# Performance work log

Hardware: AMD Instinct MI355X
Metric: run time of the kernel (lower is better)

Reference implementation:

```python
import jax, jax.numpy as jnp
import numpy as np

B, T, D = 32, 1024, 1024
PCA_DIM = 256
NS = 4
NC = 1024
SEC = PCA_DIM // NS


def setup_inputs() -> dict:
    key = jax.random.key(0)
    k1, k2, k3 = jax.random.split(key, 3)
    inputs = jax.random.normal(k1, (B, T, D), dtype=jnp.float32)
    # variance_scaling(1.0, 'fan_avg', 'normal'): std = sqrt(2 / (fan_in + fan_out))
    pca_proj = jax.random.normal(k2, (D, PCA_DIM), dtype=jnp.float32) * np.float32(np.sqrt(2.0 / (D + PCA_DIM)))
    pre_bias = jnp.zeros((1, D), dtype=jnp.float32)
    # per-section codebooks, variance_scaling(0.1, 'fan_avg', 'normal')
    codebooks = jax.random.normal(k3, (NS, NC, SEC), dtype=jnp.float32) * np.float32(np.sqrt(0.1 * 2.0 / (NC + SEC)))
    return {"inputs": inputs, "pca_proj": pca_proj, "pre_bias": pre_bias, "codebooks": codebooks}


def reference(inputs, pca_proj, pre_bias, codebooks):
    in_shape = inputs.shape
    d = in_shape[-1]
    flat = inputs.reshape(-1, d)  # [N, D]
    n = flat.shape[0]
    # --- PCA projection + reconstruction / decorrelation losses ---
    projected = (flat + pre_bias) @ pca_proj            # [N, P]
    unprojected = projected @ pca_proj.T - pre_bias     # [N, D]
    l2_loss = jnp.mean(jnp.sqrt(jnp.sum(jnp.square(flat - unprojected), axis=-1)))
    cov = projected.T @ projected / n                   # [P, P]
    cov_loss = jnp.mean(jnp.square(cov - jnp.eye(pca_proj.shape[1], dtype=projected.dtype)))
    pca_loss = l2_loss + cov_loss
    # --- per-section vector quantization ---
    ns, nc, sec = codebooks.shape
    secs = projected.reshape(n, ns, sec).transpose(1, 0, 2)  # [ns, N, sec] == jnp.split along -1

    def quantize_section(x, cb):
        # x: [N, sec], cb: [nc, sec]; squared-L2 cdist via expansion
        dist = (jnp.sum(x * x, axis=1, keepdims=True)
                - 2.0 * (x @ cb.T)
                + jnp.sum(cb * cb, axis=1)[None, :])    # [N, nc]
        idx = jnp.argmin(dist, axis=1)                  # [N]
        q = cb[idx]                                     # gather == one_hot @ cb
        loss = jnp.square(q - jax.lax.stop_gradient(x))  # [N, sec]
        q_st = x + jax.lax.stop_gradient(q - x)         # straight-through
        return q_st, loss, idx

    q, sec_loss, idx = jax.vmap(quantize_section)(secs, codebooks)  # [ns,N,sec] x2, [ns,N]
    quantized = q.transpose(1, 0, 2).reshape(n, ns * sec)           # concat sections -> [N, P]
    quantized = (quantized @ pca_proj.T - pre_bias).reshape(in_shape)  # pca_unproject
    nn_idx = idx.reshape((ns,) + in_shape[:-1])                     # [ns, B, T]
    quantization_loss = jnp.mean(sec_loss.reshape((ns,) + in_shape[:-1] + (sec,)), axis=0) + pca_loss
    codebook = jax.lax.stop_gradient(codebooks.reshape(ns * nc, sec))
    cluster_counts = jnp.ones((ns, nc), dtype=jnp.float32)  # eval mode: jnp.ones init, no EMA
    return quantized, quantization_loss, nn_idx, codebook, cluster_counts
```

## Files before the change

kernel.cpp:

```cpp
#include <hip/hip_runtime.h>
#include <math.h>

#define NROW 32768
#define DIM  1024
#define PDIM 256
#define NSEC 4
#define NCODE 1024
#define SECD 64

__global__ __launch_bounds__(256) void k_proj(const float* __restrict__ X,
                                              const float* __restrict__ W,
                                              const float* __restrict__ bias,
                                              float* __restrict__ proj) {
    __shared__ float As[16][128];
    __shared__ float Bs[16][128];
    const int t = threadIdx.x;
    const int ry = t >> 4;
    const int rx = t & 15;
    const int rb = blockIdx.y * 128;
    const int cb = blockIdx.x * 128;
    const int lr = t >> 1;
    const int lk = (t & 1) * 8;
    const int bk = t >> 4;
    const int bc = (t & 15) * 8;
    float acc[8][8] = {};
    float part[8][8] = {};
    for (int kc = 0; kc < DIM; kc += 16) {
        if (kc == 384) {
            #pragma unroll
            for (int i = 0; i < 8; ++i)
                #pragma unroll
                for (int j = 0; j < 8; ++j) { part[i][j] = acc[i][j]; acc[i][j] = 0.0f; }
        } else if (kc == 768) {
            #pragma unroll
            for (int i = 0; i < 8; ++i)
                #pragma unroll
                for (int j = 0; j < 8; ++j) { part[i][j] = __fadd_rn(part[i][j], acc[i][j]); acc[i][j] = 0.0f; }
        }
        float4 a0 = *(const float4*)&X[(size_t)(rb + lr) * DIM + kc + lk];
        float4 a1 = *(const float4*)&X[(size_t)(rb + lr) * DIM + kc + lk + 4];
        float4 c0 = *(const float4*)&bias[kc + lk];
        float4 c1 = *(const float4*)&bias[kc + lk + 4];
        a0.x += c0.x; a0.y += c0.y; a0.z += c0.z; a0.w += c0.w;
        a1.x += c1.x; a1.y += c1.y; a1.z += c1.z; a1.w += c1.w;
        float4 b0 = *(const float4*)&W[(size_t)(kc + bk) * PDIM + cb + bc];
        float4 b1 = *(const float4*)&W[(size_t)(kc + bk) * PDIM + cb + bc + 4];
        As[lk + 0][lr] = a0.x; As[lk + 1][lr] = a0.y; As[lk + 2][lr] = a0.z; As[lk + 3][lr] = a0.w;
        As[lk + 4][lr] = a1.x; As[lk + 5][lr] = a1.y; As[lk + 6][lr] = a1.z; As[lk + 7][lr] = a1.w;
        *(float4*)&Bs[bk][bc] = b0;
        *(float4*)&Bs[bk][bc + 4] = b1;
        __syncthreads();
        #pragma unroll
        for (int k = 0; k < 16; ++k) {
            float4 x0 = *(const float4*)&As[k][ry * 8];
            float4 x1 = *(const float4*)&As[k][ry * 8 + 4];
            float4 y0 = *(const float4*)&Bs[k][rx * 8];
            float4 y1 = *(const float4*)&Bs[k][rx * 8 + 4];
            float aa[8] = {x0.x, x0.y, x0.z, x0.w, x1.x, x1.y, x1.z, x1.w};
            float bb[8] = {y0.x, y0.y, y0.z, y0.w, y1.x, y1.y, y1.z, y1.w};
            #pragma unroll
            for (int i = 0; i < 8; ++i)
                #pragma unroll
                for (int j = 0; j < 8; ++j)
                    acc[i][j] = fmaf(aa[i], bb[j], acc[i][j]);
        }
        __syncthreads();
    }
    #pragma unroll
    for (int i = 0; i < 8; ++i) {
        float r[8];
        #pragma unroll
        for (int j = 0; j < 8; ++j) r[j] = __fadd_rn(part[i][j], acc[i][j]);
        const size_t base = (size_t)(rb + ry * 8 + i) * PDIM + cb + rx * 8;
        *(float4*)&proj[base]     = make_float4(r[0], r[1], r[2], r[3]);
        *(float4*)&proj[base + 4] = make_float4(r[4], r[5], r[6], r[7]);
    }
}

__global__ __launch_bounds__(256) void k_pm(const float* __restrict__ P,
                                            const float* __restrict__ M,
                                            float* __restrict__ PM) {
    __shared__ float As[16][128];
    __shared__ float Bs[16][128];
    const int t = threadIdx.x;
    const int ry = t >> 4;
    const int rx = t & 15;
    const int rb = blockIdx.y * 128;
    const int cb = blockIdx.x * 128;
    const int lr = t >> 1;
    const int lk = (t & 1) * 8;
    const int bk = t >> 4;
    const int bc = (t & 15) * 8;
    float acc[8][8] = {};
    for (int kc = 0; kc < PDIM; kc += 16) {
        float4 a0 = *(const float4*)&P[(size_t)(rb + lr) * PDIM + kc + lk];
        float4 a1 = *(const float4*)&P[(size_t)(rb + lr) * PDIM + kc + lk + 4];
        float4 b0 = *(const float4*)&M[(size_t)(kc + bk) * PDIM + cb + bc];
        float4 b1 = *(const float4*)&M[(size_t)(kc + bk) * PDIM + cb + bc + 4];
        As[lk + 0][lr] = a0.x; As[lk + 1][lr] = a0.y; As[lk + 2][lr] = a0.z; As[lk + 3][lr] = a0.w;
        As[lk + 4][lr] = a1.x; As[lk + 5][lr] = a1.y; As[lk + 6][lr] = a1.z; As[lk + 7][lr] = a1.w;
        *(float4*)&Bs[bk][bc] = b0;
        *(float4*)&Bs[bk][bc + 4] = b1;
        __syncthreads();
        #pragma unroll
        for (int k = 0; k < 16; ++k) {
            float4 x0 = *(const float4*)&As[k][ry * 8];
            float4 x1 = *(const float4*)&As[k][ry * 8 + 4];
            float4 y0 = *(const float4*)&Bs[k][rx * 8];
            float4 y1 = *(const float4*)&Bs[k][rx * 8 + 4];
            float aa[8] = {x0.x, x0.y, x0.z, x0.w, x1.x, x1.y, x1.z, x1.w};
            float bb[8] = {y0.x, y0.y, y0.z, y0.w, y1.x, y1.y, y1.z, y1.w};
            #pragma unroll
            for (int i = 0; i < 8; ++i)
                #pragma unroll
                for (int j = 0; j < 8; ++j)
                    acc[i][j] = fmaf(aa[i], bb[j], acc[i][j]);
        }
        __syncthreads();
    }
    #pragma unroll
    for (int i = 0; i < 8; ++i) {
        const size_t base = (size_t)(rb + ry * 8 + i) * PDIM + cb + rx * 8;
        *(float4*)&PM[base]     = make_float4(acc[i][0], acc[i][1], acc[i][2], acc[i][3]);
        *(float4*)&PM[base + 4] = make_float4(acc[i][4], acc[i][5], acc[i][6], acc[i][7]);
    }
}

__global__ __launch_bounds__(256) void k_wtw(const float* __restrict__ W,
                                             float* __restrict__ M) {
    __shared__ float As[16][64];
    __shared__ float Bs[16][64];
    const int t = threadIdx.x;
    const int tx = t & 15, ty = t >> 4;
    const int ib = blockIdx.x * 64;
    const int jb = blockIdx.y * 64;
    const int sk = t >> 4;
    const int sc = (t & 15) * 4;
    float acc[4][4] = {};
    for (int kc = 0; kc < DIM; kc += 16) {
        float4 a = *(const float4*)&W[(size_t)(kc + sk) * PDIM + ib + sc];
        float4 b = *(const float4*)&W[(size_t)(kc + sk) * PDIM + jb + sc];
        *(float4*)&As[sk][sc] = a;
        *(float4*)&Bs[sk][sc] = b;
        __syncthreads();
        #pragma unroll
        for (int k = 0; k < 16; ++k) {
            float4 a4 = *(const float4*)&As[k][ty * 4];
            float4 b4 = *(const float4*)&Bs[k][tx * 4];
            float aa[4] = {a4.x, a4.y, a4.z, a4.w};
            float bb[4] = {b4.x, b4.y, b4.z, b4.w};
            #pragma unroll
            for (int i = 0; i < 4; ++i)
                #pragma unroll
                for (int j = 0; j < 4; ++j)
                    acc[i][j] = fmaf(aa[i], bb[j], acc[i][j]);
        }
        __syncthreads();
    }
    #pragma unroll
    for (int i = 0; i < 4; ++i)
        #pragma unroll
        for (int j = 0; j < 4; ++j)
            M[(size_t)(ib + ty * 4 + i) * PDIM + jb + tx * 4 + j] = acc[i][j];
}

__global__ __launch_bounds__(256) void k_xn2(const float* __restrict__ X,
                                             const float* __restrict__ bias,
                                             float* __restrict__ xn2) {
    const int n = blockIdx.x * 4 + (threadIdx.x >> 6);
    const int lane = threadIdx.x & 63;
    float s = 0.0f;
    #pragma unroll
    for (int i = 0; i < 4; ++i) {
        float4 x = *(const float4*)&X[(size_t)n * DIM + i * 256 + lane * 4];
        float4 b = *(const float4*)&bias[i * 256 + lane * 4];
        float vx = x.x + b.x, vy = x.y + b.y, vz = x.z + b.z, vw = x.w + b.w;
        s = fmaf(vx, vx, s); s = fmaf(vy, vy, s);
        s = fmaf(vz, vz, s); s = fmaf(vw, vw, s);
    }
    #pragma unroll
    for (int o = 1; o < 64; o <<= 1) s += __shfl_xor(s, o);
    if (lane == 0) xn2[n] = s;
}

__global__ __launch_bounds__(256) void k_rowres(const float* __restrict__ P,
                                                const float* __restrict__ PM,
                                                const float* __restrict__ xn2,
                                                float* __restrict__ rowres) {
    const int n = blockIdx.x * 4 + (threadIdx.x >> 6);
    const int lane = threadIdx.x & 63;
    float4 p  = *(const float4*)&P[(size_t)n * PDIM + lane * 4];
    float4 pm = *(const float4*)&PM[(size_t)n * PDIM + lane * 4];
    float s = 0.0f;
    s = fmaf(p.x, pm.x - 2.0f * p.x, s);
    s = fmaf(p.y, pm.y - 2.0f * p.y, s);
    s = fmaf(p.z, pm.z - 2.0f * p.z, s);
    s = fmaf(p.w, pm.w - 2.0f * p.w, s);
    #pragma unroll
    for (int o = 1; o < 64; o <<= 1) s += __shfl_xor(s, o);
    if (lane == 0) rowres[n] = xn2[n] + s;
}

__global__ __launch_bounds__(256) void k_cov(const float* __restrict__ Pm,
                                             float* __restrict__ cov) {
    __shared__ float As[16][64];
    __shared__ float Bs[16][64];
    const int t = threadIdx.x;
    const int tx = t & 15, ty = t >> 4;
    const int ib = blockIdx.x * 64;
    const int jb = blockIdx.y * 64;
    const int nb = blockIdx.z * 2048;
    const int sk = t >> 4;
    const int sc = (t & 15) * 4;
    float acc[4][4] = {};
    for (int kc = 0; kc < 2048; kc += 16) {
        float4 a = *(const float4*)&Pm[(size_t)(nb + kc + sk) * PDIM + ib + sc];
        float4 b = *(const float4*)&Pm[(size_t)(nb + kc + sk) * PDIM + jb + sc];
        *(float4*)&As[sk][sc] = a;
        *(float4*)&Bs[sk][sc] = b;
        __syncthreads();
        #pragma unroll
        for (int k = 0; k < 16; ++k) {
            float4 a4 = *(const float4*)&As[k][ty * 4];
            float4 b4 = *(const float4*)&Bs[k][tx * 4];
            float aa[4] = {a4.x, a4.y, a4.z, a4.w};
            float bb[4] = {b4.x, b4.y, b4.z, b4.w};
            #pragma unroll
            for (int i = 0; i < 4; ++i)
                #pragma unroll
                for (int j = 0; j < 4; ++j)
                    acc[i][j] = fmaf(aa[i], bb[j], acc[i][j]);
        }
        __syncthreads();
    }
    #pragma unroll
    for (int i = 0; i < 4; ++i)
        #pragma unroll
        for (int j = 0; j < 4; ++j)
            atomicAdd(&cov[(size_t)(ib + ty * 4 + i) * PDIM + jb + tx * 4 + j], acc[i][j]);
}

__global__ __launch_bounds__(256) void k_covloss(const float* __restrict__ cov,
                                                 float* __restrict__ scal) {
    const int t = threadIdx.x;
    float s = 0.0f;
    for (int e = t; e < PDIM * PDIM; e += 256) {
        int i = e >> 8, j = e & 255;
        float v = cov[e] * (1.0f / 32768.0f) - (i == j ? 1.0f : 0.0f);
        s = fmaf(v, v, s);
    }
    #pragma unroll
    for (int o = 1; o < 64; o <<= 1) s += __shfl_xor(s, o);
    __shared__ float r4[4];
    if ((t & 63) == 0) r4[t >> 6] = s;
    __syncthreads();
    if (t == 0) scal[1] = (r4[0] + r4[1] + r4[2] + r4[3]) * (1.0f / 65536.0f);
}

__global__ __launch_bounds__(256) void k_l2(const float* __restrict__ rowres,
                                            float* __restrict__ scal) {
    int r = blockIdx.x * 256 + threadIdx.x;
    float v = sqrtf(rowres[r]);
    #pragma unroll
    for (int o = 1; o < 64; o <<= 1) v += __shfl_xor(v, o);
    if ((threadIdx.x & 63) == 0) atomicAdd(&scal[0], v);
}

__global__ __launch_bounds__(256) void k_cnorm(const float* __restrict__ cbs,
                                               float* __restrict__ cnorm) {
    int c = blockIdx.x * 256 + threadIdx.x;
    const float* p = &cbs[(size_t)c * SECD];
    float a[8];
    #pragma unroll
    for (int j = 0; j < 8; ++j) a[j] = __fmul_rn(p[j], p[j]);
    #pragma unroll
    for (int i = 8; i < 64; i += 8)
        #pragma unroll
        for (int j = 0; j < 8; ++j)
            a[j] = __fadd_rn(a[j], __fmul_rn(p[i + j], p[i + j]));
    float r = __fadd_rn(__fadd_rn(__fadd_rn(a[0], a[1]), __fadd_rn(a[2], a[3])),
                        __fadd_rn(__fadd_rn(a[4], a[5]), __fadd_rn(a[6], a[7])));
    cnorm[c] = r;
}

__global__ __launch_bounds__(256) void k_vq(const float* __restrict__ proj,
                                            const float* __restrict__ cbs,
                                            const float* __restrict__ cnorm,
                                            int* __restrict__ widx,
                                            float* __restrict__ out_idx,
                                            float* __restrict__ out_qloss) {
    __shared__ float xs[64][64];
    __shared__ float cs[64][128];
    __shared__ float xnorm[64];
    __shared__ int   sidx[64];
    const int t = threadIdx.x;
    const int ry = t >> 5;
    const int tx = t & 31;
    const int rb = blockIdx.x * 64;
    const int lr = t >> 2;
    const int kq = (t & 3) * 16;
    const int cr = t >> 1;
    const int ko = (t & 1) * 32;
    float qacc[16];
    #pragma unroll
    for (int i = 0; i < 16; ++i) qacc[i] = 0.0f;

    for (int s = 0; s < NSEC; ++s) {
        #pragma unroll
        for (int i = 0; i < 16; i += 4) {
            float4 v = *(const float4*)&proj[(size_t)(rb + lr) * PDIM + s * SECD + kq + i];
            xs[kq + i + 0][lr] = v.x; xs[kq + i + 1][lr] = v.y;
            xs[kq + i + 2][lr] = v.z; xs[kq + i + 3][lr] = v.w;
        }
        __syncthreads();
        if (t < 64) {
            float a[8];
            #pragma unroll
            for (int j = 0; j < 8; ++j) { float v = xs[j][t]; a[j] = __fmul_rn(v, v); }
            #pragma unroll
            for (int i = 8; i < 64; i += 8)
                #pragma unroll
                for (int j = 0; j < 8; ++j) {
                    float v = xs[i + j][t];
                    a[j] = __fadd_rn(a[j], __fmul_rn(v, v));
                }
            xnorm[t] = __fadd_rn(__fadd_rn(__fadd_rn(a[0], a[1]), __fadd_rn(a[2], a[3])),
                                 __fadd_rn(__fadd_rn(a[4], a[5]), __fadd_rn(a[6], a[7])));
        }
        float best[8]; int bidx[8];
        #pragma unroll
        for (int i = 0; i < 8; ++i) { best[i] = 3.4e38f; bidx[i] = 0; }

        for (int ct = 0; ct < 8; ++ct) {
            __syncthreads();
            #pragma unroll
            for (int u = 0; u < 32; u += 4) {
                float4 v = *(const float4*)&cbs[(size_t)(s * NCODE + ct * 128 + cr) * SECD + ko + u];
                cs[ko + u + 0][cr] = v.x; cs[ko + u + 1][cr] = v.y;
                cs[ko + u + 2][cr] = v.z; cs[ko + u + 3][cr] = v.w;
            }
            __syncthreads();
            float4 cn4 = *(const float4*)&cnorm[s * NCODE + ct * 128 + tx * 4];
            float cna[4] = {cn4.x, cn4.y, cn4.z, cn4.w};
            float acc[8][4] = {};
            #pragma unroll 8
            for (int k = 0; k < 64; ++k) {
                float4 x0 = *(const float4*)&xs[k][ry * 8];
                float4 x1 = *(const float4*)&xs[k][ry * 8 + 4];
                float4 b4 = *(const float4*)&cs[k][tx * 4];
                float aa[8] = {x0.x, x0.y, x0.z, x0.w, x1.x, x1.y, x1.z, x1.w};
                float bb[4] = {b4.x, b4.y, b4.z, b4.w};
                #pragma unroll
                for (int i = 0; i < 8; ++i)
                    #pragma unroll
                    for (int j = 0; j < 4; ++j)
                        acc[i][j] = fmaf(aa[i], bb[j], acc[i][j]);
            }
            #pragma unroll
            for (int i = 0; i < 8; ++i) {
                float xn = xnorm[ry * 8 + i];
                #pragma unroll
                for (int j = 0; j < 4; ++j) {
                    float d = __fadd_rn(__fsub_rn(xn, __fmul_rn(2.0f, acc[i][j])), cna[j]);
                    int code = ct * 128 + tx * 4 + j;
                    if (d < best[i]) { best[i] = d; bidx[i] = code; }
                }
            }
        }
        #pragma unroll
        for (int i = 0; i < 8; ++i) {
            float d = best[i]; int ix = bidx[i];
            #pragma unroll
            for (int o = 1; o < 32; o <<= 1) {
                float od = __shfl_xor(d, o);
                int   oi = __shfl_xor(ix, o);
                if (od < d || (od == d && oi < ix)) { d = od; ix = oi; }
            }
            if (tx == 0) {
                int row = rb + ry * 8 + i;
                widx[s * NROW + row] = ix;
                out_idx[s * NROW + row] = (float)ix;
                sidx[ry * 8 + i] = ix;
            }
        }
        __syncthreads();
        {
            const float* crow = &cbs[(size_t)(s * NCODE + sidx[lr]) * SECD];
            #pragma unroll
            for (int i = 0; i < 16; i += 4) {
                float4 q = *(const float4*)&crow[kq + i];
                float qq[4] = {q.x, q.y, q.z, q.w};
                #pragma unroll
                for (int u = 0; u < 4; ++u) {
                    float d = qq[u] - xs[kq + i + u][lr];
                    qacc[i + u] = fmaf(d, d, qacc[i + u]);
                }
            }
        }
        __syncthreads();
    }
    #pragma unroll
    for (int i = 0; i < 16; i += 4) {
        float4 v = make_float4(0.25f * qacc[i + 0], 0.25f * qacc[i + 1],
                               0.25f * qacc[i + 2], 0.25f * qacc[i + 3]);
        *(float4*)&out_qloss[(size_t)(rb + lr) * SECD + kq + i] = v;
    }
}

__global__ __launch_bounds__(256) void k_cbu(const float* __restrict__ cbs,
                                             const float* __restrict__ W,
                                             float* __restrict__ cbu) {
    __shared__ float As[16][64];
    __shared__ float Bs[16][64];
    const int t = threadIdx.x;
    const int tx = t & 15, ty = t >> 4;
    const int s = blockIdx.z;
    const int cbase = blockIdx.y * 64;
    const int db = blockIdx.x * 64;
    const int lr = t >> 2;
    const int lk = (t & 3) * 4;
    float acc[4][4] = {};
    for (int kc = 0; kc < SECD; kc += 16) {
        float4 a = *(const float4*)&cbs[(size_t)(s * NCODE + cbase + lr) * SECD + kc + lk];
        float4 b = *(const float4*)&W[(size_t)(db + lr) * PDIM + s * SECD + kc + lk];
        As[lk + 0][lr] = a.x; As[lk + 1][lr] = a.y;
        As[lk + 2][lr] = a.z; As[lk + 3][lr] = a.w;
        Bs[lk + 0][lr] = b.x; Bs[lk + 1][lr] = b.y;
        Bs[lk + 2][lr] = b.z; Bs[lk + 3][lr] = b.w;
        __syncthreads();
        #pragma unroll
        for (int k = 0; k < 16; ++k) {
            float4 a4 = *(const float4*)&As[k][ty * 4];
            float4 b4 = *(const float4*)&Bs[k][tx * 4];
            float aa[4] = {a4.x, a4.y, a4.z, a4.w};
            float bb[4] = {b4.x, b4.y, b4.z, b4.w};
            #pragma unroll
            for (int i = 0; i < 4; ++i)
                #pragma unroll
                for (int j = 0; j < 4; ++j)
                    acc[i][j] = fmaf(aa[i], bb[j], acc[i][j]);
        }
        __syncthreads();
    }
    #pragma unroll
    for (int i = 0; i < 4; ++i) {
        float4 v = make_float4(acc[i][0], acc[i][1], acc[i][2], acc[i][3]);
        *(float4*)&cbu[(size_t)(s * NCODE + cbase + ty * 4 + i) * DIM + db + tx * 4] = v;
    }
}

__global__ __launch_bounds__(256) void k_gather(const float* __restrict__ cbu,
                                                const int* __restrict__ widx,
                                                const float* __restrict__ bias,
                                                float* __restrict__ out0) {
    const int n = blockIdx.x;
    const int d = threadIdx.x * 4;
    int i0 = widx[0 * NROW + n];
    int i1 = widx[1 * NROW + n];
    int i2 = widx[2 * NROW + n];
    int i3 = widx[3 * NROW + n];
    float4 v0 = *(const float4*)&cbu[((size_t)(0 * NCODE + i0)) * DIM + d];
    float4 v1 = *(const float4*)&cbu[((size_t)(1 * NCODE + i1)) * DIM + d];
    float4 v2 = *(const float4*)&cbu[((size_t)(2 * NCODE + i2)) * DIM + d];
    float4 v3 = *(const float4*)&cbu[((size_t)(3 * NCODE + i3)) * DIM + d];
    float4 b = *(const float4*)&bias[d];
    float4 r;
    r.x = v0.x + v1.x + v2.x + v3.x - b.x;
    r.y = v0.y + v1.y + v2.y + v3.y - b.y;
    r.z = v0.z + v1.z + v2.z + v3.z - b.z;
    r.w = v0.w + v1.w + v2.w + v3.w - b.w;
    *(float4*)&out0[(size_t)n * DIM + d] = r;
}

__global__ __launch_bounds__(256) void k_addpca(float* __restrict__ out1,
                                                const float* __restrict__ scal) {
    float pca = scal[0] * (1.0f / 32768.0f) + scal[1];
    int e = blockIdx.x * 256 + threadIdx.x;
    float4* p = (float4*)out1;
    float4 v = p[e];
    v.x += pca; v.y += pca; v.z += pca; v.w += pca;
    p[e] = v;
}

__global__ __launch_bounds__(256) void k_tail(const float* __restrict__ cbs,
                                              float* __restrict__ out3,
                                              float* __restrict__ out4) {
    int e = blockIdx.x * 256 + threadIdx.x;
    ((float4*)out3)[e] = ((const float4*)cbs)[e];
    if (e < 4096) out4[e] = 1.0f;
}

extern "C" void kernel_launch(void* const* d_in, const int* in_sizes, int n_in,
                              void* d_out, int out_size, void* d_ws, size_t ws_size,
                              hipStream_t stream) {
    (void)in_sizes; (void)n_in; (void)out_size; (void)ws_size;
    const float* X    = (const float*)d_in[0];
    const float* W    = (const float*)d_in[1];
    const float* bias = (const float*)d_in[2];
    const float* cbs  = (const float*)d_in[3];

    float* out  = (float*)d_out;
    float* out0 = out;
    float* out1 = out + 33554432;
    float* out2 = out + 35651584;
    float* out3 = out + 35782656;
    float* out4 = out + 36044800;

    char* ws = (char*)d_ws;
    float* cbu    = (float*)(ws);
    float* rowres = (float*)(ws + 16777216);
    float* cov    = (float*)(ws + 16908288);
    float* scal   = (float*)(ws + 17170432);
    float* cnorm  = (float*)(ws + 17170496);
    int*   widx   = (int*)  (ws + 17186880);
    float* wtw    = (float*)(ws + 17711168);

    float* proj = out0;
    float* PM   = out0 + 16777216;
    float* xn2  = out0 + 25165824;

    hipMemsetAsync(ws + 16908288, 0, 262144 + 64, stream);

    k_proj    <<<dim3(2, 256),    256, 0, stream>>>(X, W, bias, proj);
    k_xn2     <<<8192,            256, 0, stream>>>(X, bias, xn2);
    k_wtw     <<<dim3(4, 4),      256, 0, stream>>>(W, wtw);
    k_cov     <<<dim3(4, 4, 16),  256, 0, stream>>>(proj, cov);
    k_covloss <<<1,               256, 0, stream>>>(cov, scal);
    k_pm      <<<dim3(2, 256),    256, 0, stream>>>(proj, wtw, PM);
    k_rowres  <<<8192,            256, 0, stream>>>(proj, PM, xn2, rowres);
    k_l2      <<<128,             256, 0, stream>>>(rowres, scal);
    k_cnorm   <<<16,              256, 0, stream>>>(cbs, cnorm);
    k_vq      <<<512,             256, 0, stream>>>(proj, cbs, cnorm, widx, out2, out1);
    k_cbu     <<<dim3(16, 16, 4), 256, 0, stream>>>(cbs, W, cbu);
    k_gather  <<<32768,           256, 0, stream>>>(cbu, widx, bias, out0);
    k_addpca  <<<2048,            256, 0, stream>>>(out1, scal);
    k_tail    <<<256,             256, 0, stream>>>(cbs, out3, out4);
}
```

Baseline: 1.265 ms.

## Split projection GEMM over K into three partial launches and fuse row norms

The projection GEMM is split along K into three chunks (384/384/256), each written to its own partial buffer from a third grid dimension, and a new combine kernel sums them in the same order as the old in-register partial sums. This triples the block count of the skinny GEMM, which previously had only 512 blocks, so more of the GPU is occupied. The kernel also register-prefetches the next K tile before the inner loop, and it computes the row squared norms from the tiles it already loads, using atomics, which removes the separate xn2 pass over X. The costs are extra partial-buffer writes and reads, an extra launch, and atomic float accumulation whose summation order is nondeterministic.

```diff
diff --git a/kernel.cpp b/kernel.cpp
--- a/kernel.cpp
+++ b/kernel.cpp
@@ -8,10 +8,13 @@
 #define NCODE 1024
 #define SECD 64
 
-__global__ __launch_bounds__(256) void k_proj(const float* __restrict__ X,
-                                              const float* __restrict__ W,
-                                              const float* __restrict__ bias,
-                                              float* __restrict__ proj) {
+__global__ __launch_bounds__(256, 4) void k_proj_split(const float* __restrict__ X,
+                                                       const float* __restrict__ W,
+                                                       const float* __restrict__ bias,
+                                                       float* __restrict__ S0,
+                                                       float* __restrict__ S1,
+                                                       float* __restrict__ S2,
+                                                       float* __restrict__ xn2) {
     __shared__ float As[16][128];
     __shared__ float Bs[16][128];
     const int t = threadIdx.x;
@@ -19,37 +22,53 @@
     const int rx = t & 15;
     const int rb = blockIdx.y * 128;
     const int cb = blockIdx.x * 128;
+    const int zi = blockIdx.z;
+    const int k0 = zi * 384;
+    const int klen = (zi == 2) ? 256 : 384;
+    float* __restrict__ dst = (zi == 0) ? S0 : (zi == 1 ? S1 : S2);
     const int lr = t >> 1;
     const int lk = (t & 1) * 8;
     const int bk = t >> 4;
     const int bc = (t & 15) * 8;
+    const bool do_xn = (cb == 0);
     float acc[8][8] = {};
-    float part[8][8] = {};
-    for (int kc = 0; kc < DIM; kc += 16) {
-        if (kc == 384) {
-            #pragma unroll
-            for (int i = 0; i < 8; ++i)
-                #pragma unroll
-                for (int j = 0; j < 8; ++j) { part[i][j] = acc[i][j]; acc[i][j] = 0.0f; }
-        } else if (kc == 768) {
-            #pragma unroll
-            for (int i = 0; i < 8; ++i)
-                #pragma unroll
-                for (int j = 0; j < 8; ++j) { part[i][j] = __fadd_rn(part[i][j], acc[i][j]); acc[i][j] = 0.0f; }
-        }
-        float4 a0 = *(const float4*)&X[(size_t)(rb + lr) * DIM + kc + lk];
-        float4 a1 = *(const float4*)&X[(size_t)(rb + lr) * DIM + kc + lk + 4];
-        float4 c0 = *(const float4*)&bias[kc + lk];
-        float4 c1 = *(const float4*)&bias[kc + lk + 4];
+    float xsum = 0.0f;
+    float4 a0, a1, b0, b1;
+    {
+        const float* xp = &X[(size_t)(rb + lr) * DIM + k0 + lk];
+        a0 = *(const float4*)xp;
+        a1 = *(const float4*)(xp + 4);
+        float4 c0 = *(const float4*)&bias[k0 + lk];
+        float4 c1 = *(const float4*)&bias[k0 + lk + 4];
         a0.x += c0.x; a0.y += c0.y; a0.z += c0.z; a0.w += c0.w;
         a1.x += c1.x; a1.y += c1.y; a1.z += c1.z; a1.w += c1.w;
-        float4 b0 = *(const float4*)&W[(size_t)(kc + bk) * PDIM + cb + bc];
-        float4 b1 = *(const float4*)&W[(size_t)(kc + bk) * PDIM + cb + bc + 4];
+        b0 = *(const float4*)&W[(size_t)(k0 + bk) * PDIM + cb + bc];
+        b1 = *(const float4*)&W[(size_t)(k0 + bk) * PDIM + cb + bc + 4];
+    }
+    for (int kc = 0; kc < klen; kc += 16) {
         As[lk + 0][lr] = a0.x; As[lk + 1][lr] = a0.y; As[lk + 2][lr] = a0.z; As[lk + 3][lr] = a0.w;
         As[lk + 4][lr] = a1.x; As[lk + 5][lr] = a1.y; As[lk + 6][lr] = a1.z; As[lk + 7][lr] = a1.w;
         *(float4*)&Bs[bk][bc] = b0;
         *(float4*)&Bs[bk][bc + 4] = b1;
-        __syncthreads();
+        if (do_xn) {
+            xsum = fmaf(a0.x, a0.x, xsum); xsum = fmaf(a0.y, a0.y, xsum);
+            xsum = fmaf(a0.z, a0.z, xsum); xsum = fmaf(a0.w, a0.w, xsum);
+            xsum = fmaf(a1.x, a1.x, xsum); xsum = fmaf(a1.y, a1.y, xsum);
+            xsum = fmaf(a1.z, a1.z, xsum); xsum = fmaf(a1.w, a1.w, xsum);
+        }
+        __syncthreads();
+        if (kc + 16 < klen) {
+            const int kn = k0 + kc + 16;
+            const float* xp = &X[(size_t)(rb + lr) * DIM + kn + lk];
+            a0 = *(const float4*)xp;
+            a1 = *(const float4*)(xp + 4);
+            float4 c0 = *(const float4*)&bias[kn + lk];
+            float4 c1 = *(const float4*)&bias[kn + lk + 4];
+            a0.x += c0.x; a0.y += c0.y; a0.z += c0.z; a0.w += c0.w;
+            a1.x += c1.x; a1.y += c1.y; a1.z += c1.z; a1.w += c1.w;
+            b0 = *(const float4*)&W[(size_t)(kn + bk) * PDIM + cb + bc];
+            b1 = *(const float4*)&W[(size_t)(kn + bk) * PDIM + cb + bc + 4];
+        }
         #pragma unroll
         for (int k = 0; k < 16; ++k) {
             float4 x0 = *(const float4*)&As[k][ry * 8];
@@ -68,13 +87,29 @@
     }
     #pragma unroll
     for (int i = 0; i < 8; ++i) {
-        float r[8];
-        #pragma unroll
-        for (int j = 0; j < 8; ++j) r[j] = __fadd_rn(part[i][j], acc[i][j]);
         const size_t base = (size_t)(rb + ry * 8 + i) * PDIM + cb + rx * 8;
-        *(float4*)&proj[base]     = make_float4(r[0], r[1], r[2], r[3]);
-        *(float4*)&proj[base + 4] = make_float4(r[4], r[5], r[6], r[7]);
-    }
+        *(float4*)&dst[base]     = make_float4(acc[i][0], acc[i][1], acc[i][2], acc[i][3]);
+        *(float4*)&dst[base + 4] = make_float4(acc[i][4], acc[i][5], acc[i][6], acc[i][7]);
+    }
+    if (do_xn) {
+        xsum += __shfl_xor(xsum, 1);
+        if ((t & 1) == 0) atomicAdd(&xn2[rb + lr], xsum);
+    }
+}
+
+__global__ __launch_bounds__(256) void k_combine(const float* __restrict__ S1,
+                                                 const float* __restrict__ S2,
+                                                 float* __restrict__ P) {
+    int e = blockIdx.x * 256 + threadIdx.x;
+    float4 s0 = ((const float4*)P)[e];
+    float4 s1 = ((const float4*)S1)[e];
+    float4 s2 = ((const float4*)S2)[e];
+    float4 r;
+    r.x = __fadd_rn(__fadd_rn(s0.x, s1.x), s2.x);
+    r.y = __fadd_rn(__fadd_rn(s0.y, s1.y), s2.y);
+    r.z = __fadd_rn(__fadd_rn(s0.z, s1.z), s2.z);
+    r.w = __fadd_rn(__fadd_rn(s0.w, s1.w), s2.w);
+    ((float4*)P)[e] = r;
 }
 
 __global__ __launch_bounds__(256) void k_pm(const float* __restrict__ P,
@@ -162,25 +197,6 @@
         #pragma unroll
         for (int j = 0; j < 4; ++j)
             M[(size_t)(ib + ty * 4 + i) * PDIM + jb + tx * 4 + j] = acc[i][j];
-}
-
-__global__ __launch_bounds__(256) void k_xn2(const float* __restrict__ X,
-                                             const float* __restrict__ bias,
-                                             float* __restrict__ xn2) {
-    const int n = blockIdx.x * 4 + (threadIdx.x >> 6);
-    const int lane = threadIdx.x & 63;
-    float s = 0.0f;
-    #pragma unroll
-    for (int i = 0; i < 4; ++i) {
-        float4 x = *(const float4*)&X[(size_t)n * DIM + i * 256 + lane * 4];
-        float4 b = *(const float4*)&bias[i * 256 + lane * 4];
-        float vx = x.x + b.x, vy = x.y + b.y, vz = x.z + b.z, vw = x.w + b.w;
-        s = fmaf(vx, vx, s); s = fmaf(vy, vy, s);
-        s = fmaf(vz, vz, s); s = fmaf(vw, vw, s);
-    }
-    #pragma unroll
-    for (int o = 1; o < 64; o <<= 1) s += __shfl_xor(s, o);
-    if (lane == 0) xn2[n] = s;
 }
 
 __global__ __launch_bounds__(256) void k_rowres(const float* __restrict__ P,
@@ -511,28 +527,30 @@
     float* rowres = (float*)(ws + 16777216);
     float* cov    = (float*)(ws + 16908288);
     float* scal   = (float*)(ws + 17170432);
-    float* cnorm  = (float*)(ws + 17170496);
-    int*   widx   = (int*)  (ws + 17186880);
-    float* wtw    = (float*)(ws + 17711168);
+    float* xn2    = (float*)(ws + 17170496);
+    float* cnorm  = (float*)(ws + 17301568);
+    int*   widx   = (int*)  (ws + 17317952);
+    float* wtw    = (float*)(ws + 17842240);
 
     float* proj = out0;
-    float* PM   = out0 + 16777216;
-    float* xn2  = out0 + 25165824;
-
-    hipMemsetAsync(ws + 16908288, 0, 262144 + 64, stream);
-
-    k_proj    <<<dim3(2, 256),    256, 0, stream>>>(X, W, bias, proj);
-    k_xn2     <<<8192,            256, 0, stream>>>(X, bias, xn2);
-    k_wtw     <<<dim3(4, 4),      256, 0, stream>>>(W, wtw);
-    k_cov     <<<dim3(4, 4, 16),  256, 0, stream>>>(proj, cov);
-    k_covloss <<<1,               256, 0, stream>>>(cov, scal);
-    k_pm      <<<dim3(2, 256),    256, 0, stream>>>(proj, wtw, PM);
-    k_rowres  <<<8192,            256, 0, stream>>>(proj, PM, xn2, rowres);
-    k_l2      <<<128,             256, 0, stream>>>(rowres, scal);
-    k_cnorm   <<<16,              256, 0, stream>>>(cbs, cnorm);
-    k_vq      <<<512,             256, 0, stream>>>(proj, cbs, cnorm, widx, out2, out1);
-    k_cbu     <<<dim3(16, 16, 4), 256, 0, stream>>>(cbs, W, cbu);
-    k_gather  <<<32768,           256, 0, stream>>>(cbu, widx, bias, out0);
-    k_addpca  <<<2048,            256, 0, stream>>>(out1, scal);
-    k_tail    <<<256,             256, 0, stream>>>(cbs, out3, out4);
-}
+    float* S1   = out0 + 8388608;
+    float* S2   = out0 + 16777216;
+    float* PM   = out0 + 25165824;
+
+    hipMemsetAsync(ws + 16908288, 0, 262144 + 64 + 131072, stream);
+
+    k_proj_split<<<dim3(2, 256, 3), 256, 0, stream>>>(X, W, bias, proj, S1, S2, xn2);
+    k_combine   <<<8192,            256, 0, stream>>>(S1, S2, proj);
+    k_wtw       <<<dim3(4, 4),      256, 0, stream>>>(W, wtw);
+    k_cov       <<<dim3(4, 4, 16),  256, 0, stream>>>(proj, cov);
+    k_covloss   <<<1,               256, 0, stream>>>(cov, scal);
+    k_pm        <<<dim3(2, 256),    256, 0, stream>>>(proj, wtw, PM);
+    k_rowres    <<<8192,            256, 0, stream>>>(proj, PM, xn2, rowres);
+    k_l2        <<<128,             256, 0, stream>>>(rowres, scal);
+    k_cnorm     <<<16,              256, 0, stream>>>(cbs, cnorm);
+    k_vq        <<<512,             256, 0, stream>>>(proj, cbs, cnorm, widx, out2, out1);
+    k_cbu       <<<dim3(16, 16, 4), 256, 0, stream>>>(cbs, W, cbu);
+    k_gather    <<<32768,           256, 0, stream>>>(cbu, widx, bias, out0);
+    k_addpca    <<<2048,            256, 0, stream>>>(out1, scal);
+    k_tail      <<<256,             256, 0, stream>>>(cbs, out3, out4);
+}
```

Result: slower. 2.092 ms (+65.3%).
